# Optimization experiments

Hardware: AMD Instinct MI355X
Metric: run time of the kernel (lower is better)

## Reference

```python
import jax, jax.numpy as jnp
import numpy as np
import math

H = 8          # num heads
HID = 768      # LM hidden size
FFN = 3072     # 4 * HID
EOUT = 256     # final embed_dim
EPS = 1e-5


def layernorm(x, g, b):
    m = jnp.mean(x, axis=-1, keepdims=True)
    v = jnp.mean((x - m) ** 2, axis=-1, keepdims=True)
    return (x - m) * jax.lax.rsqrt(v + EPS) * g + b


def _masked_softmax(logits, mask):
    # logits: (b, h, s); mask: (b, s) bool
    logits = jnp.where(mask[:, None, :], logits, -10000.0)
    return jax.nn.softmax(logits, axis=-1)


def fast_attention(x, mask, wq, bq, wk, bk, wv, bv, wo, bo):
    b, s, e = x.shape
    d = e // H
    scale = math.sqrt(d)
    # (b, h, s, d)
    q = (x @ wq + bq).reshape(b, s, H, d).transpose(0, 2, 1, 3)
    k = (x @ wk + bk).reshape(b, s, H, d).transpose(0, 2, 1, 3)
    v = (x @ wv + bv).reshape(b, s, H, d).transpose(0, 2, 1, 3)
    q_w = _masked_softmax(q.sum(-1) / scale, mask)            # (b,h,s)
    q_global = jnp.einsum('bhs,bhsd->bhd', q_w, q)            # (b,h,d)
    k_w = _masked_softmax(jnp.einsum('bhsd,bhd->bhs', k, q_global), mask)
    k_global = jnp.einsum('bhs,bhsd->bhd', k_w, k)
    v_w = _masked_softmax(jnp.einsum('bhsd,bhd->bhs', q, k_global), mask)
    attn_out = v_w[..., None] * v                              # (b,h,s,d)
    attn_out = attn_out.transpose(0, 2, 1, 3).reshape(b, s, e)
    return attn_out @ wo + bo


def fast_pooling(x, mask, wq, bq, wk, bk, wv, bv, wo, bo, ng, nb):
    b, s, e = x.shape
    d = e // H
    scale = math.sqrt(d)
    q = (x @ wq + bq).reshape(b, s, H, d).transpose(0, 2, 1, 3)
    k = (x @ wk + bk).reshape(b, s, H, d).transpose(0, 2, 1, 3)
    v = (x @ wv + bv).reshape(b, s, H, d).transpose(0, 2, 1, 3)
    q_w = _masked_softmax(q.sum(-1) / scale, mask)
    q_global = jnp.einsum('bhs,bhsd->bhd', q_w, q)
    k_w = _masked_softmax(jnp.einsum('bhsd,bhd->bhs', k, q_global), mask)
    k_global = jnp.einsum('bhs,bhsd->bhd', k_w, k)
    v_w = _masked_softmax(jnp.einsum('bhsd,bhd->bhs', q, k_global), mask)
    v_global = jnp.einsum('bhs,bhsd->bhd', v_w, v)            # (b,h,d)
    fused = jnp.concatenate([q_global, v_global], axis=-1)    # (b,h,2d)
    # torch: fused.transpose(1,2).view(b, 2e)  -> layout (b, 2d, h) flattened
    fused = jnp.swapaxes(fused, 1, 2).reshape(b, 2 * e)
    out = fused @ wo + bo
    residual = jnp.swapaxes(q_global, 1, 2).reshape(b, e)
    return layernorm(out + residual, ng, nb)


def setup_inputs() -> dict:
    key = jax.random.key(0)
    ks = iter(jax.random.split(key, 64))
    B, S = 1024, 64

    def w(shape, scale=0.02):
        return jax.random.normal(next(ks), shape, dtype=jnp.float32) * scale

    inp = {
        'token_states': jax.random.normal(next(ks), (B, S, HID), dtype=jnp.float32),
        'attention_mask': jnp.ones((B, S), dtype=jnp.int32),
        # FastformerBlock (1 layer)
        'l_n1_g': jnp.ones((HID,), jnp.float32), 'l_n1_b': jnp.zeros((HID,), jnp.float32),
        'l_wq': w((HID, HID)), 'l_bq': jnp.zeros((HID,), jnp.float32),
        'l_wk': w((HID, HID)), 'l_bk': jnp.zeros((HID,), jnp.float32),
        'l_wv': w((HID, HID)), 'l_bv': jnp.zeros((HID,), jnp.float32),
        'l_wo': w((HID, HID)), 'l_bo': jnp.zeros((HID,), jnp.float32),
        'l_n2_g': jnp.ones((HID,), jnp.float32), 'l_n2_b': jnp.zeros((HID,), jnp.float32),
        'l_w1': w((HID, FFN)), 'l_b1': jnp.zeros((FFN,), jnp.float32),
        'l_w2': w((FFN, HID)), 'l_b2': jnp.zeros((HID,), jnp.float32),
        # FastformerPooling
        'p_wq': w((HID, HID)), 'p_bq': jnp.zeros((HID,), jnp.float32),
        'p_wk': w((HID, HID)), 'p_bk': jnp.zeros((HID,), jnp.float32),
        'p_wv': w((HID, HID)), 'p_bv': jnp.zeros((HID,), jnp.float32),
        'p_wo': w((2 * HID, HID)), 'p_bo': jnp.zeros((HID,), jnp.float32),
        'p_ng': jnp.ones((HID,), jnp.float32), 'p_nb': jnp.zeros((HID,), jnp.float32),
        # token_norm, proj, out_norm
        'tn_g': jnp.ones((HID,), jnp.float32), 'tn_b': jnp.zeros((HID,), jnp.float32),
        'proj_w': w((HID, EOUT)), 'proj_b': jnp.zeros((EOUT,), jnp.float32),
        'on_g': jnp.ones((EOUT,), jnp.float32), 'on_b': jnp.zeros((EOUT,), jnp.float32),
    }
    return inp


def reference(token_states, attention_mask,
              l_n1_g, l_n1_b, l_wq, l_bq, l_wk, l_bk, l_wv, l_bv, l_wo, l_bo,
              l_n2_g, l_n2_b, l_w1, l_b1, l_w2, l_b2,
              p_wq, p_bq, p_wk, p_bk, p_wv, p_bv, p_wo, p_bo, p_ng, p_nb,
              tn_g, tn_b, proj_w, proj_b, on_g, on_b):
    mask = attention_mask != 0
    x = token_states
    # FastformerBlock
    x = x + fast_attention(layernorm(x, l_n1_g, l_n1_b), mask,
                           l_wq, l_bq, l_wk, l_bk, l_wv, l_bv, l_wo, l_bo)
    h = layernorm(x, l_n2_g, l_n2_b)
    x = x + (jax.nn.gelu(h @ l_w1 + l_b1, approximate=False) @ l_w2 + l_b2)
    # Pooling + head
    pooled = fast_pooling(x, mask, p_wq, p_bq, p_wk, p_bk, p_wv, p_bv,
                          p_wo, p_bo, p_ng, p_nb)
    pooled = layernorm(pooled, tn_g, tn_b)
    news_vec = pooled @ proj_w + proj_b
    return layernorm(news_vec, on_g, on_b)
```

## Files before the change

kernel.cpp:

```cpp
#include <hip/hip_runtime.h>
#include <math.h>

#define NHEAD 8
#define HID   768
#define FFND  3072
#define EOUTD 256
#define BATCH 1024
#define TOK   (BATCH*64)

#define EPI_RESF  1
#define EPI_RESB  2
#define EPI_GELU  4
#define EPI_OUTF  8
#define EPI_OUTB  16

typedef __attribute__((ext_vector_type(8))) short short8;
typedef __attribute__((ext_vector_type(4))) float f32x4;

#define AS1 __attribute__((address_space(1)))
#define AS3 __attribute__((address_space(3)))

__device__ __forceinline__ void async16(const void* g, void* l) {
  __builtin_amdgcn_global_load_lds(
      (AS1 unsigned int*)(unsigned long long)g,
      (AS3 unsigned int*)(unsigned int)(unsigned long long)l,
      16, 0, 0);
}

__device__ __forceinline__ float bf2f(unsigned short u) {
  union { unsigned int i; float f; } c; c.i = ((unsigned int)u) << 16; return c.f;
}
__device__ __forceinline__ unsigned short f2bf(float f) {
  union { float f; unsigned int i; } c; c.f = f;
  unsigned int x = c.i + 0x7fffu + ((c.i >> 16) & 1u);
  return (unsigned short)(x >> 16);
}
__device__ __forceinline__ float wsum(float v) {
#pragma unroll
  for (int o = 32; o > 0; o >>= 1) v += __shfl_xor(v, o);
  return v;
}
__device__ __forceinline__ float gelu_f(float v) {
  const float z = fabsf(v) * 0.70710678118654752f;
  const float t = 1.0f / (1.0f + 0.3275911f * z);
  const float poly = t * (0.254829592f + t * (-0.284496736f +
                     t * (1.421413741f + t * (-1.453152027f + t * 1.061405429f))));
  float erfv = 1.0f - poly * __expf(-z * z);
  erfv = (v < 0.f) ? -erfv : erfv;
  return 0.5f * v * (1.0f + erfv);
}

template<int EPI>
__global__ __launch_bounds__(256, 3) void gemm_k(
    const unsigned short* __restrict__ A, const unsigned short* __restrict__ Wt,
    const float* __restrict__ bias,
    const float* __restrict__ residF, const unsigned short* __restrict__ residB,
    float* __restrict__ outF, unsigned short* __restrict__ outB,
    int M, int N, int K)
{
  __shared__ unsigned short lA[128 * 64];
  __shared__ unsigned short lB[128 * 64];
  const int tid  = threadIdx.x;

  const int nT  = N >> 7;
  const int per = gridDim.x >> 3;
  const int tile = (blockIdx.x & 7) * per + (blockIdx.x >> 3);
  int m_idx = tile / nT;
  int n_idx = tile - m_idx * nT;
  if (m_idx & 1) n_idx = nT - 1 - n_idx;
  const int n0 = n_idx * 128;
  const int m0 = m_idx * 128;

  const int lane = tid & 63;
  const int wid  = tid >> 6;
  const int wm   = wid & 1, wn = wid >> 1;
  const int m16  = lane & 15, quad = lane >> 4;

  f32x4 zero = {0.0f, 0.0f, 0.0f, 0.0f};
  f32x4 acc[4][4];
#pragma unroll
  for (int i = 0; i < 4; i++)
#pragma unroll
    for (int j = 0; j < 4; j++) acc[i][j] = zero;

  long aoff[4], boff[4];
#pragma unroll
  for (int j = 0; j < 4; j++) {
    const int L = tid + j * 256;
    const int row = L >> 3;
    const int kc  = (L & 7) ^ (row & 7);
    aoff[j] = (long)(m0 + row) * K + kc * 8;
    boff[j] = (long)(n0 + row) * K + kc * 8;
  }

  for (int k0 = 0; k0 < K; k0 += 64) {
#pragma unroll
    for (int j = 0; j < 4; j++)
      async16(A + aoff[j] + k0, lA + (size_t)(j * 256 + wid * 64) * 8);
#pragma unroll
    for (int j = 0; j < 4; j++)
      async16(Wt + boff[j] + k0, lB + (size_t)(j * 256 + wid * 64) * 8);
    __syncthreads();
#pragma unroll
    for (int s = 0; s < 2; s++) {
      short8 af[4], bfr[4];
#pragma unroll
      for (int mi = 0; mi < 4; mi++) {
        const int row = wm * 64 + mi * 16 + m16;
        const int kc  = (s * 4 + quad) ^ (row & 7);
        af[mi] = *(const short8*)(lA + row * 64 + kc * 8);
      }
#pragma unroll
      for (int ni = 0; ni < 4; ni++) {
        const int row = wn * 64 + ni * 16 + m16;
        const int kc  = (s * 4 + quad) ^ (row & 7);
        bfr[ni] = *(const short8*)(lB + row * 64 + kc * 8);
      }
#pragma unroll
      for (int mi = 0; mi < 4; mi++)
#pragma unroll
        for (int ni = 0; ni < 4; ni++)
          acc[mi][ni] = __builtin_amdgcn_mfma_f32_16x16x32_bf16(bfr[ni], af[mi], acc[mi][ni], 0, 0, 0);
    }
    __syncthreads();
  }

#pragma unroll
  for (int mi = 0; mi < 4; mi++) {
    const int m = m0 + wm * 64 + mi * 16 + m16;
    const long rb = (long)m * N;
#pragma unroll
    for (int ni = 0; ni < 4; ni++) {
      const int nb = n0 + wn * 64 + ni * 16 + quad * 4;
      f32x4 v = acc[mi][ni];
      const f32x4 bi = *(const f32x4*)(bias + nb);
#pragma unroll
      for (int r = 0; r < 4; r++) v[r] += bi[r];
      if (EPI & EPI_RESF) {
        const f32x4 rf = *(const f32x4*)(residF + rb + nb);
#pragma unroll
        for (int r = 0; r < 4; r++) v[r] += rf[r];
      }
      if (EPI & EPI_RESB) {
        const unsigned long long rv = *(const unsigned long long*)(residB + rb + nb);
#pragma unroll
        for (int r = 0; r < 4; r++) v[r] += bf2f((unsigned short)(rv >> (16 * r)));
      }
      if (EPI & EPI_GELU) {
#pragma unroll
        for (int r = 0; r < 4; r++) v[r] = gelu_f(v[r]);
      }
      if (EPI & EPI_OUTF) *(f32x4*)(outF + rb + nb) = v;
      if (EPI & EPI_OUTB) {
        unsigned long long o = 0;
#pragma unroll
        for (int r = 0; r < 4; r++) o |= (unsigned long long)f2bf(v[r]) << (16 * r);
        *(unsigned long long*)(outB + rb + nb) = o;
      }
    }
  }
}

template<bool POOL>
__global__ __launch_bounds__(256) void fastattn2_k(
    const unsigned short* __restrict__ Q,
    const unsigned short* __restrict__ Kx,
    const unsigned short* __restrict__ V,
    int ld,
    const int* __restrict__ mask,
    unsigned short* __restrict__ attnO,
    unsigned short* __restrict__ fused,
    float* __restrict__ qres)
{
  const int lane = threadIdx.x & 63;
  const int wid  = threadIdx.x >> 6;
  const int gw   = blockIdx.x * 4 + wid;
  const int b = gw >> 3, h = gw & 7;
  const int c = lane & 15, quad = lane >> 4;
  const unsigned short* Qp = Q  + (long)b * 64 * ld + h * 96;
  const unsigned short* Kp = Kx + (long)b * 64 * ld + h * 96;
  const unsigned short* Vp = V  + (long)b * 64 * ld + h * 96;
  const float mval = (mask[b * 64 + lane] != 0) ? 1.0f : 0.0f;

  f32x4 G[4][4];
  f32x4 zero = {0.f, 0.f, 0.f, 0.f};
#pragma unroll
  for (int mi = 0; mi < 4; mi++)
#pragma unroll
    for (int ni = 0; ni < 4; ni++) G[mi][ni] = zero;
  float ql[4] = {0.f, 0.f, 0.f, 0.f};

#pragma unroll
  for (int kc = 0; kc < 3; kc++) {
    const int dcol = kc * 32 + quad * 8;
    short8 afr[4], bfr[4];
#pragma unroll
    for (int mi = 0; mi < 4; mi++)
      afr[mi] = *(const short8*)(Kp + (long)(mi * 16 + c) * ld + dcol);
#pragma unroll
    for (int ni = 0; ni < 4; ni++)
      bfr[ni] = *(const short8*)(Qp + (long)(ni * 16 + c) * ld + dcol);
#pragma unroll
    for (int ni = 0; ni < 4; ni++) {
      float t = 0.f;
#pragma unroll
      for (int j = 0; j < 8; j++) t += bf2f((unsigned short)bfr[ni][j]);
      ql[ni] += t;
    }
#pragma unroll
    for (int mi = 0; mi < 4; mi++)
#pragma unroll
      for (int ni = 0; ni < 4; ni++)
        G[mi][ni] = __builtin_amdgcn_mfma_f32_16x16x32_bf16(afr[mi], bfr[ni], G[mi][ni], 0, 0, 0);
  }
#pragma unroll
  for (int ni = 0; ni < 4; ni++) {
    ql[ni] += __shfl_xor(ql[ni], 16);
    ql[ni] += __shfl_xor(ql[ni], 32);
  }

  float qw[4];
  {
    float lg[4], mx = -3.4e38f;
#pragma unroll
    for (int ni = 0; ni < 4; ni++) {
      const float mk = __shfl(mval, ni * 16 + c);
      lg[ni] = (mk > 0.5f) ? ql[ni] * 0.102062072615966f : -10000.0f;
      mx = fmaxf(mx, lg[ni]);
    }
#pragma unroll
    for (int o = 1; o <= 8; o <<= 1) mx = fmaxf(mx, __shfl_xor(mx, o));
    float se = 0.f;
#pragma unroll
    for (int ni = 0; ni < 4; ni++) { qw[ni] = expf(lg[ni] - mx); se += qw[ni]; }
#pragma unroll
    for (int o = 1; o <= 8; o <<= 1) se += __shfl_xor(se, o);
    const float inv = 1.0f / se;
#pragma unroll
    for (int ni = 0; ni < 4; ni++) qw[ni] *= inv;
  }

  float kw[16];
#pragma unroll
  for (int mi = 0; mi < 4; mi++)
#pragma unroll
    for (int r = 0; r < 4; r++) {
      float a = 0.f;
#pragma unroll
      for (int ni = 0; ni < 4; ni++) a += G[mi][ni][r] * qw[ni];
      kw[mi * 4 + r] = a;
    }
#pragma unroll
  for (int i = 0; i < 16; i++)
#pragma unroll
    for (int o = 1; o <= 8; o <<= 1) kw[i] += __shfl_xor(kw[i], o);

  {
    float mx2 = -3.4e38f;
#pragma unroll
    for (int i = 0; i < 16; i++) {
      const int mi = i >> 2, r = i & 3;
      const float mk = __shfl(mval, mi * 16 + quad * 4 + r);
      kw[i] = (mk > 0.5f) ? kw[i] : -10000.0f;
      mx2 = fmaxf(mx2, kw[i]);
    }
    mx2 = fmaxf(mx2, __shfl_xor(mx2, 16));
    mx2 = fmaxf(mx2, __shfl_xor(mx2, 32));
    float se2 = 0.f;
#pragma unroll
    for (int i = 0; i < 16; i++) { kw[i] = expf(kw[i] - mx2); se2 += kw[i]; }
    se2 += __shfl_xor(se2, 16);
    se2 += __shfl_xor(se2, 32);
    const float inv = 1.0f / se2;
#pragma unroll
    for (int i = 0; i < 16; i++) kw[i] *= inv;
  }

  float vw[4];
  {
    float vl[4] = {0.f, 0.f, 0.f, 0.f};
#pragma unroll
    for (int ni = 0; ni < 4; ni++) {
#pragma unroll
      for (int mi = 0; mi < 4; mi++)
#pragma unroll
        for (int r = 0; r < 4; r++) vl[ni] += G[mi][ni][r] * kw[mi * 4 + r];
      vl[ni] += __shfl_xor(vl[ni], 16);
      vl[ni] += __shfl_xor(vl[ni], 32);
    }
    float mx = -3.4e38f;
#pragma unroll
    for (int ni = 0; ni < 4; ni++) {
      const float mk = __shfl(mval, ni * 16 + c);
      vl[ni] = (mk > 0.5f) ? vl[ni] : -10000.0f;
      mx = fmaxf(mx, vl[ni]);
    }
#pragma unroll
    for (int o = 1; o <= 8; o <<= 1) mx = fmaxf(mx, __shfl_xor(mx, o));
    float se = 0.f;
#pragma unroll
    for (int ni = 0; ni < 4; ni++) { vw[ni] = expf(vl[ni] - mx); se += vw[ni]; }
#pragma unroll
    for (int o = 1; o <= 8; o <<= 1) se += __shfl_xor(se, o);
    const float inv = 1.0f / se;
#pragma unroll
    for (int ni = 0; ni < 4; ni++) vw[ni] *= inv;
  }

  if (!POOL) {
    __shared__ float swv[4][64];
    if (quad == 0) {
#pragma unroll
      for (int ni = 0; ni < 4; ni++) swv[wid][ni * 16 + c] = vw[ni];
    }
    __syncthreads();
    unsigned short* Op = attnO + (long)b * 64 * 768 + h * 96;
#pragma unroll
    for (int it = 0; it < 12; it++) {
      const int idx = it * 64 + lane;
      const int s = idx / 12, cw = idx % 12;
      short8 v = *(const short8*)(Vp + (long)s * ld + cw * 8);
      const float w = swv[wid][s];
      short8 o;
#pragma unroll
      for (int j = 0; j < 8; j++) o[j] = (short)f2bf(w * bf2f((unsigned short)v[j]));
      *(short8*)(Op + (long)s * 768 + cw * 8) = o;
    }
  } else {
    float qg[24], vg[24];
#pragma unroll
    for (int kc = 0; kc < 3; kc++) {
      const int dcol = kc * 32 + quad * 8;
      short8 fq[4], fv[4];
#pragma unroll
      for (int ni = 0; ni < 4; ni++) {
        fq[ni] = *(const short8*)(Qp + (long)(ni * 16 + c) * ld + dcol);
        fv[ni] = *(const short8*)(Vp + (long)(ni * 16 + c) * ld + dcol);
      }
#pragma unroll
      for (int j = 0; j < 8; j++) {
        float aq = 0.f, av = 0.f;
#pragma unroll
        for (int ni = 0; ni < 4; ni++) {
          aq += qw[ni] * bf2f((unsigned short)fq[ni][j]);
          av += vw[ni] * bf2f((unsigned short)fv[ni][j]);
        }
        qg[kc * 8 + j] = aq; vg[kc * 8 + j] = av;
      }
    }
#pragma unroll
    for (int i = 0; i < 24; i++) {
#pragma unroll
      for (int o = 1; o <= 8; o <<= 1) {
        qg[i] += __shfl_xor(qg[i], o);
        vg[i] += __shfl_xor(vg[i], o);
      }
    }
    if (c == 0) {
#pragma unroll
      for (int kc = 0; kc < 3; kc++)
#pragma unroll
        for (int j = 0; j < 8; j++) {
          const int d = kc * 32 + quad * 8 + j;
          const float qv = qg[kc * 8 + j], vv = vg[kc * 8 + j];
          fused[(long)b * 1536 + d * 8 + h]        = f2bf(qv);
          fused[(long)b * 1536 + (96 + d) * 8 + h] = f2bf(vv);
          qres[(long)b * 768 + d * 8 + h] = qv;
        }
    }
  }
}

__global__ __launch_bounds__(256) void ln768_k(
    const float* __restrict__ x, const float* __restrict__ g, const float* __restrict__ b,
    unsigned short* __restrict__ out)
{
  const int tid = threadIdx.x;
  const long row = blockIdx.x;
  const float* xr = x + row * 768;
  const float v0 = xr[tid], v1 = xr[tid + 256], v2 = xr[tid + 512];
  __shared__ float red[4];
  const int wid = tid >> 6, ln = tid & 63;
  float s = wsum(v0 + v1 + v2);
  if (ln == 0) red[wid] = s;
  __syncthreads();
  const float mean = (red[0] + red[1] + red[2] + red[3]) * (1.0f / 768.0f);
  __syncthreads();
  const float d0 = v0 - mean, d1 = v1 - mean, d2 = v2 - mean;
  float q = wsum(d0 * d0 + d1 * d1 + d2 * d2);
  if (ln == 0) red[wid] = q;
  __syncthreads();
  const float var = (red[0] + red[1] + red[2] + red[3]) * (1.0f / 768.0f);
  const float rs = rsqrtf(var + 1e-5f);
  unsigned short* o = out + row * 768;
  o[tid]       = f2bf(d0 * rs * g[tid]       + b[tid]);
  o[tid + 256] = f2bf(d1 * rs * g[tid + 256] + b[tid + 256]);
  o[tid + 512] = f2bf(d2 * rs * g[tid + 512] + b[tid + 512]);
}

__global__ __launch_bounds__(256) void ln768b_k(
    const unsigned short* __restrict__ x, const float* __restrict__ g, const float* __restrict__ b,
    unsigned short* __restrict__ out)
{
  const int tid = threadIdx.x;
  const long row = blockIdx.x;
  const unsigned short* xr = x + row * 768;
  const float v0 = bf2f(xr[tid]), v1 = bf2f(xr[tid + 256]), v2 = bf2f(xr[tid + 512]);
  __shared__ float red[4];
  const int wid = tid >> 6, ln = tid & 63;
  float s = wsum(v0 + v1 + v2);
  if (ln == 0) red[wid] = s;
  __syncthreads();
  const float mean = (red[0] + red[1] + red[2] + red[3]) * (1.0f / 768.0f);
  __syncthreads();
  const float d0 = v0 - mean, d1 = v1 - mean, d2 = v2 - mean;
  float q = wsum(d0 * d0 + d1 * d1 + d2 * d2);
  if (ln == 0) red[wid] = q;
  __syncthreads();
  const float var = (red[0] + red[1] + red[2] + red[3]) * (1.0f / 768.0f);
  const float rs = rsqrtf(var + 1e-5f);
  unsigned short* o = out + row * 768;
  o[tid]       = f2bf(d0 * rs * g[tid]       + b[tid]);
  o[tid + 256] = f2bf(d1 * rs * g[tid + 256] + b[tid + 256]);
  o[tid + 512] = f2bf(d2 * rs * g[tid + 512] + b[tid + 512]);
}

__global__ __launch_bounds__(256) void ln2x_k(
    const float* __restrict__ x,
    const float* __restrict__ g1, const float* __restrict__ b1,
    const float* __restrict__ g2, const float* __restrict__ b2,
    unsigned short* __restrict__ out)
{
  const int tid = threadIdx.x;
  const long row = blockIdx.x;
  const float* xr = x + row * 768;
  const float v0 = xr[tid], v1 = xr[tid + 256], v2 = xr[tid + 512];
  __shared__ float red[4];
  const int wid = tid >> 6, ln = tid & 63;
  float s = wsum(v0 + v1 + v2);
  if (ln == 0) red[wid] = s;
  __syncthreads();
  const float mean = (red[0] + red[1] + red[2] + red[3]) * (1.0f / 768.0f);
  __syncthreads();
  const float d0 = v0 - mean, d1 = v1 - mean, d2 = v2 - mean;
  float q = wsum(d0 * d0 + d1 * d1 + d2 * d2);
  if (ln == 0) red[wid] = q;
  __syncthreads();
  const float var = (red[0] + red[1] + red[2] + red[3]) * (1.0f / 768.0f);
  const float rs = rsqrtf(var + 1e-5f);
  const float y0 = d0 * rs * g1[tid]       + b1[tid];
  const float y1 = d1 * rs * g1[tid + 256] + b1[tid + 256];
  const float y2 = d2 * rs * g1[tid + 512] + b1[tid + 512];
  __syncthreads();
  float s2 = wsum(y0 + y1 + y2);
  if (ln == 0) red[wid] = s2;
  __syncthreads();
  const float mean2 = (red[0] + red[1] + red[2] + red[3]) * (1.0f / 768.0f);
  __syncthreads();
  const float e0 = y0 - mean2, e1 = y1 - mean2, e2 = y2 - mean2;
  float q2 = wsum(e0 * e0 + e1 * e1 + e2 * e2);
  if (ln == 0) red[wid] = q2;
  __syncthreads();
  const float var2 = (red[0] + red[1] + red[2] + red[3]) * (1.0f / 768.0f);
  const float rs2 = rsqrtf(var2 + 1e-5f);
  unsigned short* o = out + row * 768;
  o[tid]       = f2bf(e0 * rs2 * g2[tid]       + b2[tid]);
  o[tid + 256] = f2bf(e1 * rs2 * g2[tid + 256] + b2[tid + 256]);
  o[tid + 512] = f2bf(e2 * rs2 * g2[tid + 512] + b2[tid + 512]);
}

__global__ __launch_bounds__(256) void lnf_k(
    const float* __restrict__ x, const float* __restrict__ g, const float* __restrict__ b,
    float* __restrict__ out)
{
  const int tid = threadIdx.x;
  const long row = blockIdx.x;
  const float v = x[row * 256 + tid];
  __shared__ float red[4];
  const int wid = tid >> 6, ln = tid & 63;
  float s = wsum(v);
  if (ln == 0) red[wid] = s;
  __syncthreads();
  const float mean = (red[0] + red[1] + red[2] + red[3]) * (1.0f / 256.0f);
  __syncthreads();
  const float d = v - mean;
  float q = wsum(d * d);
  if (ln == 0) red[wid] = q;
  __syncthreads();
  const float var = (red[0] + red[1] + red[2] + red[3]) * (1.0f / 256.0f);
  const float rs = rsqrtf(var + 1e-5f);
  out[row * 256 + tid] = d * rs * g[tid] + b[tid];
}

__global__ __launch_bounds__(256) void tcast_k(
    const float* __restrict__ W, unsigned short* __restrict__ Wt, int K, int N)
{
  __shared__ float t[32][33];
  const int tx = threadIdx.x & 31, ty = threadIdx.x >> 5;
  const int n0 = blockIdx.x * 32, k0 = blockIdx.y * 32;
#pragma unroll
  for (int j = 0; j < 32; j += 8)
    t[ty + j][tx] = W[(long)(k0 + ty + j) * N + n0 + tx];
  __syncthreads();
#pragma unroll
  for (int j = 0; j < 32; j += 8)
    Wt[(long)(n0 + ty + j) * K + k0 + tx] = f2bf(t[tx][ty + j]);
}

__global__ __launch_bounds__(256) void cat3_k(
    const float* __restrict__ a, const float* __restrict__ b, const float* __restrict__ c,
    float* __restrict__ dst)
{
  const int i = blockIdx.x * 256 + threadIdx.x;
  dst[i] = (i < 768) ? a[i] : (i < 1536 ? b[i - 768] : c[i - 1536]);
}

extern "C" void kernel_launch(void* const* d_in, const int* in_sizes, int n_in,
                              void* d_out, int out_size, void* d_ws, size_t ws_size,
                              hipStream_t stream)
{
  const float* x    = (const float*)d_in[0];
  const int*   mask = (const int*)d_in[1];
  const float* n1g = (const float*)d_in[2];  const float* n1b = (const float*)d_in[3];
  const float* wq  = (const float*)d_in[4];  const float* bq  = (const float*)d_in[5];
  const float* wk  = (const float*)d_in[6];  const float* bk  = (const float*)d_in[7];
  const float* wv  = (const float*)d_in[8];  const float* bv  = (const float*)d_in[9];
  const float* wo  = (const float*)d_in[10]; const float* bo  = (const float*)d_in[11];
  const float* n2g = (const float*)d_in[12]; const float* n2b = (const float*)d_in[13];
  const float* w1  = (const float*)d_in[14]; const float* b1  = (const float*)d_in[15];
  const float* w2  = (const float*)d_in[16]; const float* b2  = (const float*)d_in[17];
  const float* pwq = (const float*)d_in[18]; const float* pbq = (const float*)d_in[19];
  const float* pwk = (const float*)d_in[20]; const float* pbk = (const float*)d_in[21];
  const float* pwv = (const float*)d_in[22]; const float* pbv = (const float*)d_in[23];
  const float* pwo = (const float*)d_in[24]; const float* pbo = (const float*)d_in[25];
  const float* png = (const float*)d_in[26]; const float* pnb = (const float*)d_in[27];
  const float* tng = (const float*)d_in[28]; const float* tnb = (const float*)d_in[29];
  const float* pjw = (const float*)d_in[30]; const float* pjb = (const float*)d_in[31];
  const float* ong = (const float*)d_in[32]; const float* onb = (const float*)d_in[33];
  float* out = (float*)d_out;

  char* p = (char*)d_ws;
  auto alloc = [&](size_t n) { void* r = (void*)p; p += (n + 255) & ~(size_t)255; return r; };

  unsigned short* wqkvt = (unsigned short*)alloc((size_t)3 * HID * HID * 2);
  unsigned short* wot   = (unsigned short*)alloc((size_t)HID * HID * 2);
  unsigned short* w1t   = (unsigned short*)alloc((size_t)FFND * HID * 2);
  unsigned short* w2t   = (unsigned short*)alloc((size_t)HID * FFND * 2);
  unsigned short* pqkvt = (unsigned short*)alloc((size_t)3 * HID * HID * 2);
  unsigned short* pwot  = (unsigned short*)alloc((size_t)HID * 2 * HID * 2);
  unsigned short* pjwt  = (unsigned short*)alloc((size_t)EOUTD * HID * 2);
  float*          qkvbias = (float*)alloc((size_t)3 * HID * 4);
  float*          pqkvbias= (float*)alloc((size_t)3 * HID * 4);
  unsigned short* bfA   = (unsigned short*)alloc((size_t)TOK * HID * 2);
  unsigned short* QKVb  = (unsigned short*)alloc((size_t)TOK * 3 * HID * 2);
  unsigned short* bfB   = (unsigned short*)alloc((size_t)TOK * HID * 2);
  unsigned short* x2b   = (unsigned short*)alloc((size_t)TOK * HID * 2);
  unsigned short* fusedb= (unsigned short*)alloc((size_t)BATCH * 2 * HID * 2);
  float*          qresb = (float*)alloc((size_t)BATCH * HID * 4);
  float*          preln = (float*)alloc((size_t)BATCH * HID * 4);
  unsigned short* pooledb=(unsigned short*)alloc((size_t)BATCH * HID * 2);
  float*          news  = (float*)alloc((size_t)BATCH * EOUTD * 4);
  (void)ws_size; (void)in_sizes; (void)n_in; (void)out_size;

  tcast_k<<<dim3(HID/32,  HID/32),  256, 0, stream>>>(wq,  wqkvt,                 HID, HID);
  tcast_k<<<dim3(HID/32,  HID/32),  256, 0, stream>>>(wk,  wqkvt + (size_t)HID*HID,   HID, HID);
  tcast_k<<<dim3(HID/32,  HID/32),  256, 0, stream>>>(wv,  wqkvt + (size_t)2*HID*HID, HID, HID);
  tcast_k<<<dim3(HID/32,  HID/32),  256, 0, stream>>>(wo,  wot,  HID,  HID);
  tcast_k<<<dim3(FFND/32, HID/32),  256, 0, stream>>>(w1,  w1t,  HID,  FFND);
  tcast_k<<<dim3(HID/32,  FFND/32), 256, 0, stream>>>(w2,  w2t,  FFND, HID);
  tcast_k<<<dim3(HID/32,  HID/32),  256, 0, stream>>>(pwq, pqkvt,                 HID, HID);
  tcast_k<<<dim3(HID/32,  HID/32),  256, 0, stream>>>(pwk, pqkvt + (size_t)HID*HID,   HID, HID);
  tcast_k<<<dim3(HID/32,  HID/32),  256, 0, stream>>>(pwv, pqkvt + (size_t)2*HID*HID, HID, HID);
  tcast_k<<<dim3(HID/32,  (2*HID)/32), 256, 0, stream>>>(pwo, pwot, 2*HID, HID);
  tcast_k<<<dim3(EOUTD/32, HID/32), 256, 0, stream>>>(pjw, pjwt, HID,  EOUTD);
  cat3_k<<<9, 256, 0, stream>>>(bq,  bk,  bv,  qkvbias);
  cat3_k<<<9, 256, 0, stream>>>(pbq, pbk, pbv, pqkvbias);

  ln768_k<<<TOK, 256, 0, stream>>>(x, n1g, n1b, bfA);

  gemm_k<EPI_OUTB><<<(TOK/128)*(3*HID/128), 256, 0, stream>>>(
      bfA, wqkvt, qkvbias, nullptr, nullptr, nullptr, QKVb, TOK, 3*HID, HID);

  fastattn2_k<false><<<BATCH * NHEAD / 4, 256, 0, stream>>>(
      QKVb, QKVb + HID, QKVb + 2*HID, 3*HID, mask, bfB, nullptr, nullptr);

  gemm_k<EPI_OUTB | EPI_RESF><<<(TOK/128)*(HID/128), 256, 0, stream>>>(
      bfB, wot, bo, x, nullptr, nullptr, x2b, TOK, HID, HID);

  ln768b_k<<<TOK, 256, 0, stream>>>(x2b, n2g, n2b, bfA);

  for (int c = 0; c < 4; c++) {
    const size_t ro = (size_t)c * 16384;
    gemm_k<EPI_OUTB | EPI_GELU><<<(16384/128)*(FFND/128), 256, 0, stream>>>(
        bfA + ro * HID, w1t, b1, nullptr, nullptr, nullptr, bfB, 16384, FFND, HID);
    gemm_k<EPI_OUTB | EPI_RESB><<<(16384/128)*(HID/128), 256, 0, stream>>>(
        bfB, w2t, b2, nullptr, x2b + ro * HID, nullptr, bfA + ro * HID, 16384, HID, FFND);
  }

  gemm_k<EPI_OUTB><<<(TOK/128)*(3*HID/128), 256, 0, stream>>>(
      bfA, pqkvt, pqkvbias, nullptr, nullptr, nullptr, QKVb, TOK, 3*HID, HID);

  fastattn2_k<true><<<BATCH * NHEAD / 4, 256, 0, stream>>>(
      QKVb, QKVb + HID, QKVb + 2*HID, 3*HID, mask, nullptr, fusedb, qresb);

  gemm_k<EPI_OUTF | EPI_RESF><<<(BATCH/128)*(HID/128), 256, 0, stream>>>(
      fusedb, pwot, pbo, qresb, nullptr, preln, nullptr, BATCH, HID, 2*HID);

  ln2x_k<<<BATCH, 256, 0, stream>>>(preln, png, pnb, tng, tnb, pooledb);

  gemm_k<EPI_OUTF><<<(BATCH/128)*(EOUTD/128), 256, 0, stream>>>(
      pooledb, pjwt, pjb, nullptr, nullptr, news, nullptr, BATCH, EOUTD, HID);

  lnf_k<<<BATCH, 256, 0, stream>>>(news, ong, onb, out);
}
```

Before: 2.142 ms.

## Add 256x256-tile pipelined GEMM kernel for the large token GEMMs

Adds a new 512-thread GEMM kernel with 256x256 output tiles, 128 KB of dynamic LDS holding double-buffered A/B stages, async global-to-LDS loads interleaved with MFMA quarter-steps, explicit vmcnt waits and barriers, and raised wave priority around the MFMAs. The QKV, output-projection and FFN GEMMs switch to it. The FFN now runs in two 32768-row chunks and reuses the larger QKV buffer for its intermediate. The aim is more data reuse per byte loaded and better overlap of loads with compute, at the cost of fewer resident blocks and a hand-tuned schedule that assumes K is a multiple of 128.

```diff
diff --git a/kernel.cpp b/kernel.cpp
--- a/kernel.cpp
+++ b/kernel.cpp
@@ -50,6 +50,9 @@
   return 0.5f * v * (1.0f + erfv);
 }
 
+#define SBAR() { __builtin_amdgcn_s_barrier(); asm volatile("" ::: "memory"); }
+#define WAITV(n) asm volatile("s_waitcnt vmcnt(" #n ")" ::: "memory")
+
 template<int EPI>
 __global__ __launch_bounds__(256, 3) void gemm_k(
     const unsigned short* __restrict__ A, const unsigned short* __restrict__ Wt,
@@ -131,6 +134,186 @@
     const long rb = (long)m * N;
 #pragma unroll
     for (int ni = 0; ni < 4; ni++) {
+      const int nb = n0 + wn * 64 + ni * 16 + quad * 4;
+      f32x4 v = acc[mi][ni];
+      const f32x4 bi = *(const f32x4*)(bias + nb);
+#pragma unroll
+      for (int r = 0; r < 4; r++) v[r] += bi[r];
+      if (EPI & EPI_RESF) {
+        const f32x4 rf = *(const f32x4*)(residF + rb + nb);
+#pragma unroll
+        for (int r = 0; r < 4; r++) v[r] += rf[r];
+      }
+      if (EPI & EPI_RESB) {
+        const unsigned long long rv = *(const unsigned long long*)(residB + rb + nb);
+#pragma unroll
+        for (int r = 0; r < 4; r++) v[r] += bf2f((unsigned short)(rv >> (16 * r)));
+      }
+      if (EPI & EPI_GELU) {
+#pragma unroll
+        for (int r = 0; r < 4; r++) v[r] = gelu_f(v[r]);
+      }
+      if (EPI & EPI_OUTF) *(f32x4*)(outF + rb + nb) = v;
+      if (EPI & EPI_OUTB) {
+        unsigned long long o = 0;
+#pragma unroll
+        for (int r = 0; r < 4; r++) o |= (unsigned long long)f2bf(v[r]) << (16 * r);
+        *(unsigned long long*)(outB + rb + nb) = o;
+      }
+    }
+  }
+}
+
+template<int EPI>
+__global__ __launch_bounds__(512, 2) void gemm256_k(
+    const unsigned short* __restrict__ A, const unsigned short* __restrict__ Wt,
+    const float* __restrict__ bias,
+    const float* __restrict__ residF, const unsigned short* __restrict__ residB,
+    float* __restrict__ outF, unsigned short* __restrict__ outB,
+    int M, int N, int K)
+{
+  extern __shared__ unsigned short lds[];
+  unsigned short* lA = lds;
+  unsigned short* lB = lds + 32768;
+
+  const int tid  = threadIdx.x;
+  const int lane = tid & 63;
+  const int wid  = tid >> 6;
+
+  const int nT  = N >> 8;
+  const int per = gridDim.x >> 3;
+  const int tile = (blockIdx.x & 7) * per + (blockIdx.x >> 3);
+  int m_idx = tile / nT;
+  int n_idx = tile - m_idx * nT;
+  if (m_idx & 1) n_idx = nT - 1 - n_idx;
+  const int m0 = m_idx << 8, n0 = n_idx << 8;
+
+  const int wm = wid >> 2, wn = wid & 3;
+  const int m16 = lane & 15, quad = lane >> 4;
+
+  const int r_lo = lane >> 3;
+  const int kcg  = (lane & 7) ^ r_lo;
+  long aoffj[2], boffj[2];
+  int  ldsoj[2];
+#pragma unroll
+  for (int j = 0; j < 2; ++j) {
+    const int rr = (j * 8 + wid) * 8 + r_lo;
+    aoffj[j] = (long)(m0 + rr) * K + kcg * 8;
+    boffj[j] = (long)(n0 + rr) * K + kcg * 8;
+    ldsoj[j] = (j * 8 + wid) * 512;
+  }
+
+  auto stA = [&](int c, int hh, int t) {
+    async16(A + aoffj[0] + (long)hh * 128 * K + t * 64, lA + c * 16384 + hh * 8192 + ldsoj[0]);
+    async16(A + aoffj[1] + (long)hh * 128 * K + t * 64, lA + c * 16384 + hh * 8192 + ldsoj[1]);
+  };
+  auto stB = [&](int c, int hh, int t) {
+    async16(Wt + boffj[0] + (long)hh * 128 * K + t * 64, lB + c * 16384 + hh * 8192 + ldsoj[0]);
+    async16(Wt + boffj[1] + (long)hh * 128 * K + t * 64, lB + c * 16384 + hh * 8192 + ldsoj[1]);
+  };
+
+  const int xsw = m16 & 7;
+  const int kx0 = ((0 + quad) ^ xsw) * 8;
+  const int kx1 = ((4 + quad) ^ xsw) * 8;
+
+  f32x4 zero = {0.f, 0.f, 0.f, 0.f};
+  f32x4 acc[8][4];
+#pragma unroll
+  for (int i = 0; i < 8; i++)
+#pragma unroll
+    for (int j = 0; j < 4; j++) acc[i][j] = zero;
+
+  short8 af[4][2], bf[4][2];
+  auto ldA = [&](int c, int mh) {
+#pragma unroll
+    for (int mi = 0; mi < 4; ++mi) {
+      const unsigned short* base = lA + c * 16384 + (wm * 128 + (mh * 4 + mi) * 16 + m16) * 64;
+      af[mi][0] = *(const short8*)(base + kx0);
+      af[mi][1] = *(const short8*)(base + kx1);
+    }
+  };
+  auto ldB = [&](int c, int nh) {
+#pragma unroll
+    for (int nn = 0; nn < 2; ++nn) {
+      const unsigned short* base = lB + c * 16384 + (wn * 64 + (nh * 2 + nn) * 16 + m16) * 64;
+      bf[nh * 2 + nn][0] = *(const short8*)(base + kx0);
+      bf[nh * 2 + nn][1] = *(const short8*)(base + kx1);
+    }
+  };
+  auto mmaq = [&](int mh, int nh) {
+    __builtin_amdgcn_s_setprio(1);
+#pragma unroll
+    for (int ks = 0; ks < 2; ++ks)
+#pragma unroll
+      for (int mi = 0; mi < 4; ++mi)
+#pragma unroll
+        for (int nn = 0; nn < 2; ++nn)
+          acc[mh * 4 + mi][nh * 2 + nn] = __builtin_amdgcn_mfma_f32_16x16x32_bf16(
+              bf[nh * 2 + nn][ks], af[mi][ks], acc[mh * 4 + mi][nh * 2 + nn], 0, 0, 0);
+    __builtin_amdgcn_s_setprio(0);
+  };
+
+  const int NI = K >> 7;
+
+  stA(0, 0, 0); stA(0, 1, 0); stB(0, 0, 0); stB(0, 1, 0);
+  stB(1, 0, 1); stB(1, 1, 1);
+  WAITV(4);
+  SBAR();
+
+  for (int i = 0; i < NI - 1; ++i) {
+    const int t1 = 2 * i + 1, s0 = 2 * i + 2, s1 = 2 * i + 3;
+    ldA(0, 0); ldB(0, 0);
+    stA(1, 0, t1);
+    SBAR(); mmaq(0, 0); SBAR();
+    ldB(0, 1);
+    stA(1, 1, t1);
+    SBAR(); mmaq(0, 1); SBAR();
+    ldA(0, 1);
+    stB(0, 0, s0);
+    SBAR(); mmaq(1, 1); SBAR();
+    stB(0, 1, s0);
+    WAITV(4);
+    SBAR(); mmaq(1, 0); SBAR();
+    ldA(1, 0); ldB(1, 0);
+    stA(0, 0, s0);
+    SBAR(); mmaq(0, 0); SBAR();
+    ldB(1, 1);
+    stA(0, 1, s0);
+    SBAR(); mmaq(0, 1); SBAR();
+    ldA(1, 1);
+    stB(1, 0, s1);
+    SBAR(); mmaq(1, 1); SBAR();
+    stB(1, 1, s1);
+    WAITV(4);
+    SBAR(); mmaq(1, 0); SBAR();
+  }
+  {
+    const int t1 = 2 * NI - 1;
+    ldA(0, 0); ldB(0, 0);
+    stA(1, 0, t1);
+    SBAR(); mmaq(0, 0); SBAR();
+    ldB(0, 1);
+    stA(1, 1, t1);
+    SBAR(); mmaq(0, 1); SBAR();
+    ldA(0, 1);
+    SBAR(); mmaq(1, 1); SBAR();
+    WAITV(0);
+    SBAR(); mmaq(1, 0); SBAR();
+    ldA(1, 0); ldB(1, 0);
+    SBAR(); mmaq(0, 0); SBAR();
+    ldB(1, 1);
+    SBAR(); mmaq(0, 1); SBAR();
+    ldA(1, 1);
+    SBAR(); mmaq(1, 1); SBAR();
+    mmaq(1, 0);
+  }
+
+#pragma unroll
+  for (int mi = 0; mi < 8; ++mi) {
+    const int m = m0 + wm * 128 + mi * 16 + m16;
+    const long rb = (long)m * N;
+#pragma unroll
+    for (int ni = 0; ni < 4; ++ni) {
       const int nb = n0 + wn * 64 + ni * 16 + quad * 4;
       f32x4 v = acc[mi][ni];
       const f32x4 bi = *(const f32x4*)(bias + nb);
@@ -539,6 +722,19 @@
   const float* ong = (const float*)d_in[32]; const float* onb = (const float*)d_in[33];
   float* out = (float*)d_out;
 
+  static int lds_attr_done = 0;
+  if (!lds_attr_done) {
+    lds_attr_done = 1;
+    hipFuncSetAttribute((const void*)gemm256_k<EPI_OUTB>,
+                        hipFuncAttributeMaxDynamicSharedMemorySize, 131072);
+    hipFuncSetAttribute((const void*)gemm256_k<EPI_OUTB | EPI_RESF>,
+                        hipFuncAttributeMaxDynamicSharedMemorySize, 131072);
+    hipFuncSetAttribute((const void*)gemm256_k<EPI_OUTB | EPI_GELU>,
+                        hipFuncAttributeMaxDynamicSharedMemorySize, 131072);
+    hipFuncSetAttribute((const void*)gemm256_k<EPI_OUTB | EPI_RESB>,
+                        hipFuncAttributeMaxDynamicSharedMemorySize, 131072);
+  }
+
   char* p = (char*)d_ws;
   auto alloc = [&](size_t n) { void* r = (void*)p; p += (n + 255) & ~(size_t)255; return r; };
 
@@ -578,26 +774,26 @@
 
   ln768_k<<<TOK, 256, 0, stream>>>(x, n1g, n1b, bfA);
 
-  gemm_k<EPI_OUTB><<<(TOK/128)*(3*HID/128), 256, 0, stream>>>(
+  gemm256_k<EPI_OUTB><<<(TOK/256)*(3*HID/256), 512, 131072, stream>>>(
       bfA, wqkvt, qkvbias, nullptr, nullptr, nullptr, QKVb, TOK, 3*HID, HID);
 
   fastattn2_k<false><<<BATCH * NHEAD / 4, 256, 0, stream>>>(
       QKVb, QKVb + HID, QKVb + 2*HID, 3*HID, mask, bfB, nullptr, nullptr);
 
-  gemm_k<EPI_OUTB | EPI_RESF><<<(TOK/128)*(HID/128), 256, 0, stream>>>(
+  gemm256_k<EPI_OUTB | EPI_RESF><<<(TOK/256)*(HID/256), 512, 131072, stream>>>(
       bfB, wot, bo, x, nullptr, nullptr, x2b, TOK, HID, HID);
 
   ln768b_k<<<TOK, 256, 0, stream>>>(x2b, n2g, n2b, bfA);
 
-  for (int c = 0; c < 4; c++) {
-    const size_t ro = (size_t)c * 16384;
-    gemm_k<EPI_OUTB | EPI_GELU><<<(16384/128)*(FFND/128), 256, 0, stream>>>(
-        bfA + ro * HID, w1t, b1, nullptr, nullptr, nullptr, bfB, 16384, FFND, HID);
-    gemm_k<EPI_OUTB | EPI_RESB><<<(16384/128)*(HID/128), 256, 0, stream>>>(
-        bfB, w2t, b2, nullptr, x2b + ro * HID, nullptr, bfA + ro * HID, 16384, HID, FFND);
-  }
-
-  gemm_k<EPI_OUTB><<<(TOK/128)*(3*HID/128), 256, 0, stream>>>(
+  for (int c = 0; c < 2; c++) {
+    const size_t ro = (size_t)c * 32768;
+    gemm256_k<EPI_OUTB | EPI_GELU><<<(32768/256)*(FFND/256), 512, 131072, stream>>>(
+        bfA + ro * HID, w1t, b1, nullptr, nullptr, nullptr, QKVb, 32768, FFND, HID);
+    gemm256_k<EPI_OUTB | EPI_RESB><<<(32768/256)*(HID/256), 512, 131072, stream>>>(
+        QKVb, w2t, b2, nullptr, x2b + ro * HID, nullptr, bfA + ro * HID, 32768, HID, FFND);
+  }
+
+  gemm256_k<EPI_OUTB><<<(TOK/256)*(3*HID/256), 512, 131072, stream>>>(
       bfA, pqkvt, pqkvbias, nullptr, nullptr, nullptr, QKVb, TOK, 3*HID, HID);
 
   fastattn2_k<true><<<BATCH * NHEAD / 4, 256, 0, stream>>>(
```

Result: slower. 2.439 ms (+13.9%).
